# Kernel optimization log

Measured on AMD Instinct MI355X. Metric: run time of the kernel, lower is better.

Reference implementation:

```python
import jax, jax.numpy as jnp
import numpy as np

B, Z, K, T = 4, 64, 400, 48000
CIN, COUT, KS, DIL = 128, 128, 3, 1
H = 32


def setup_inputs() -> dict:
    key = jax.random.key(0)
    ks = jax.random.split(key, 10)
    s = lambda n: 1.0 / np.sqrt(n)
    return {
        "x": jax.random.normal(ks[0], (B, CIN, T), jnp.float32),
        "z": jax.random.normal(ks[1], (B, Z, K), jnp.float32),
        # weight_model: Conv1d(Z->H, k=1), ReLU, Conv1d(H -> CIN*COUT*KS, k=1)
        "w1": jax.random.normal(ks[2], (H, Z), jnp.float32) * s(Z),
        "b1": jax.random.normal(ks[3], (H,), jnp.float32) * 0.01,
        "w2": jax.random.normal(ks[4], (CIN * COUT * KS, H), jnp.float32) * s(H),
        "b2": jax.random.normal(ks[5], (CIN * COUT * KS,), jnp.float32) * s(CIN * KS),
        # bias_model: Conv1d(Z->H, k=1), ReLU, Conv1d(H -> COUT, k=1)
        "bw1": jax.random.normal(ks[6], (H, Z), jnp.float32) * s(Z),
        "bb1": jax.random.normal(ks[7], (H,), jnp.float32) * 0.01,
        "bw2": jax.random.normal(ks[8], (COUT, H), jnp.float32) * s(H),
        "bb2": jax.random.normal(ks[9], (COUT,), jnp.float32) * 0.01,
    }


def _mlp1x1(z, wa, ba, wb, bb):
    # two pointwise Conv1d layers with ReLU in between; z: [B, Z, K]
    h = jax.nn.relu(jnp.einsum('hz,bzk->bhk', wa, z) + ba[None, :, None])
    return jnp.einsum('oh,bhk->bok', wb, h) + bb[None, :, None]


def _unfold_causal(x, ksize, dil):
    # causal im2col: tap i is x delayed by i*dil samples (left-padded with zeros)
    pad = dil * (ksize - 1)
    xp = jnp.pad(x, ((0, 0), (0, 0), (pad, 0)))
    taps = [xp[:, :, pad - i * dil: pad - i * dil + x.shape[-1]] for i in range(ksize)]
    return jnp.concatenate(taps, axis=1)  # [B, CIN*KS, T]


def reference(x, z, w1, b1, w2, b2, bw1, bb1, bw2, bb2):
    Tk = T // K  # samples per weight chunk
    xu = _unfold_causal(x, KS, DIL)                       # [B, CIN*KS, T]
    xr = xu.transpose(0, 2, 1).reshape(B * K, Tk, CIN * KS)
    w = _mlp1x1(z, w1, b1, w2, b2)                        # [B, CIN*COUT*KS, K]
    w = w.reshape(B, CIN * KS, COUT, K).transpose(0, 3, 1, 2).reshape(B * K, CIN * KS, COUT)
    bias = _mlp1x1(z, bw1, bb1, bw2, bb2)                 # [B, COUT, K]
    bias = bias.transpose(0, 2, 1).reshape(B * K, COUT)
    y = jnp.einsum('btc,bco->bto', xr, w) + bias[:, None, :]
    return y.reshape(B, T, COUT).transpose(0, 2, 1)       # [B, COUT, T]
```

## Files before the change

kernel.cpp:

```cpp
#include <hip/hip_runtime.h>
#include <stdint.h>

#define TT     48000
#define TK     120
#define NC     128
#define NA     384
#define NZ     64
#define NH     32
#define NK     400
#define NCHUNK 1600
#define MW     49152
#define XROWS  48002

typedef float f32x4 __attribute__((ext_vector_type(4)));
typedef __bf16 bf16x8 __attribute__((ext_vector_type(8)));

static __device__ __forceinline__ uint16_t f2bf(float f) {
    uint32_t x; __builtin_memcpy(&x, &f, 4);
    return (uint16_t)((x + 0x7fffu + ((x >> 16) & 1u)) >> 16);
}
static __device__ __forceinline__ uint32_t pk2(uint16_t lo, uint16_t hi) {
    return (uint32_t)lo | ((uint32_t)hi << 16);
}

__global__ __launch_bounds__(256) void k0w(
    const float* __restrict__ w2, const float* __restrict__ b2,
    uint16_t* __restrict__ w2p, float* __restrict__ b2p) {
    int m = blockIdx.x * 256 + threadIdx.x;
    int a = m >> 7, c = m & 127;
    int mp = c * NA + a;
    const float* src = w2 + (size_t)m * NH;
    uint16_t* dst = w2p + (size_t)mp * NH;
#pragma unroll
    for (int i = 0; i < NH; i += 8) {
        float4 v0 = *(const float4*)(src + i);
        float4 v1 = *(const float4*)(src + i + 4);
        uint4 o;
        o.x = pk2(f2bf(v0.x), f2bf(v0.y));
        o.y = pk2(f2bf(v0.z), f2bf(v0.w));
        o.z = pk2(f2bf(v1.x), f2bf(v1.y));
        o.w = pk2(f2bf(v1.z), f2bf(v1.w));
        *(uint4*)(dst + i) = o;
    }
    b2p[mp] = b2[m];
}

__global__ __launch_bounds__(256) void k0x(
    const float* __restrict__ x, uint16_t* __restrict__ Xt) {
    int t0 = blockIdx.x * 128, cin0 = blockIdx.y * 64, b = blockIdx.z;
    int tid = threadIdx.x;
    __shared__ __align__(16) uint16_t Lt[128][72];
    const float* xb = x + ((size_t)b * NC + cin0) * TT + t0;
    int cg = (tid & 7) * 8;
    int tq = (tid >> 3) * 4;
    uint16_t vb[4][8];
#pragma unroll
    for (int i = 0; i < 8; ++i) {
        float4 v = *(const float4*)(xb + (size_t)(cg + i) * TT + tq);
        vb[0][i] = f2bf(v.x); vb[1][i] = f2bf(v.y);
        vb[2][i] = f2bf(v.z); vb[3][i] = f2bf(v.w);
    }
#pragma unroll
    for (int j = 0; j < 4; ++j) {
        uint4 o; __builtin_memcpy(&o, vb[j], 16);
        *(uint4*)&Lt[tq + j][cg] = o;
    }
    __syncthreads();
    uint16_t* XtB = Xt + (size_t)b * XROWS * NC;
#pragma unroll
    for (int r = 0; r < 4; ++r) {
        int s = r * 256 + tid;
        int t = s >> 3, cc = s & 7;
        uint4 o = *(uint4*)&Lt[t][cc * 8];
        *(uint4*)(XtB + (size_t)(t0 + t + 2) * NC + cin0 + cc * 8) = o;
    }
    if (blockIdx.x == 0 && blockIdx.y == 0 && tid < 32)
        *(uint4*)(XtB + tid * 8) = make_uint4(0, 0, 0, 0);
}

__global__ __launch_bounds__(256) void k1_hidden(
    const float* __restrict__ z,
    const float* __restrict__ w1, const float* __restrict__ b1,
    const float* __restrict__ bw1, const float* __restrict__ bb1,
    const float* __restrict__ bw2, const float* __restrict__ bb2,
    uint16_t* __restrict__ Hb, float* __restrict__ biasws) {
    int tid = threadIdx.x, lane = tid & 63, w = tid >> 6;
    int chunk0 = blockIdx.x * 4;
    int b = chunk0 / NK;
    int k0 = chunk0 - b * NK;

    __shared__ float w1sT[64][33];
    __shared__ float bw1sT[64][33];
    __shared__ float bw2s[128][33];
    __shared__ float zs[64][4];
    __shared__ float hbs[4][33];
    __shared__ float b1s[32], bb1s[32], bb2s[128];

    {
        int row = tid >> 3, c0 = (tid & 7) * 8;
        float4 a0 = *(const float4*)(w1 + row * NZ + c0);
        float4 a1 = *(const float4*)(w1 + row * NZ + c0 + 4);
        float4 c0v = *(const float4*)(bw1 + row * NZ + c0);
        float4 c1v = *(const float4*)(bw1 + row * NZ + c0 + 4);
        const float av[8] = {a0.x,a0.y,a0.z,a0.w,a1.x,a1.y,a1.z,a1.w};
        const float cv[8] = {c0v.x,c0v.y,c0v.z,c0v.w,c1v.x,c1v.y,c1v.z,c1v.w};
#pragma unroll
        for (int j = 0; j < 8; ++j) {
            w1sT[c0 + j][row]  = av[j];
            bw1sT[c0 + j][row] = cv[j];
        }
    }
    {
        int r = tid >> 1, cb = (tid & 1) * 16;
        float4 v0 = *(const float4*)(bw2 + r * NH + cb);
        float4 v1 = *(const float4*)(bw2 + r * NH + cb + 4);
        float4 v2 = *(const float4*)(bw2 + r * NH + cb + 8);
        float4 v3 = *(const float4*)(bw2 + r * NH + cb + 12);
        const float vv[16] = {v0.x,v0.y,v0.z,v0.w,v1.x,v1.y,v1.z,v1.w,
                              v2.x,v2.y,v2.z,v2.w,v3.x,v3.y,v3.z,v3.w};
#pragma unroll
        for (int j = 0; j < 16; ++j) bw2s[r][cb + j] = vv[j];
    }
    if (tid < 64) {
        float4 zv = *(const float4*)(z + ((size_t)b * NZ + tid) * NK + k0);
        zs[tid][0] = zv.x; zs[tid][1] = zv.y; zs[tid][2] = zv.z; zs[tid][3] = zv.w;
    }
    if (tid < 32) { b1s[tid] = b1[tid]; bb1s[tid] = bb1[tid]; }
    if (tid >= 128 && tid < 256) bb2s[tid - 128] = bb2[tid - 128];
    __syncthreads();

    int chunk = chunk0 + w;
    if (lane < NH) {
        float s = b1s[lane];
#pragma unroll
        for (int i = 0; i < NZ; ++i) s = fmaf(w1sT[i][lane], zs[i][w], s);
        Hb[(size_t)chunk * NH + lane] = f2bf(fmaxf(s, 0.f));
    } else {
        int j = lane - NH;
        float s = bb1s[j];
#pragma unroll
        for (int i = 0; i < NZ; ++i) s = fmaf(bw1sT[i][j], zs[i][w], s);
        hbs[w][j] = fmaxf(s, 0.f);
    }

#pragma unroll
    for (int r = 0; r < 2; ++r) {
        int c = r * 64 + lane;
        float s = bb2s[c];
#pragma unroll
        for (int j = 0; j < NH; ++j) s = fmaf(bw2s[c][j], hbs[w][j], s);
        biasws[(size_t)chunk * NC + c] = s;
    }
}

__global__ __launch_bounds__(256) void k2_wgen(
    const uint16_t* __restrict__ w2p, const float* __restrict__ b2p,
    const uint16_t* __restrict__ Hb, uint16_t* __restrict__ Wt,
    int chunk0, int nchunk) {
    int tid = threadIdx.x, lane = tid & 63, w = tid >> 6;
    int quad = lane >> 4, li = lane & 15;
    __shared__ __align__(16) uint16_t St[4][16][264];

    int clocal = blockIdx.y * 16 + li;
    int cl = clocal < nchunk ? clocal : (nchunk - 1);
    bf16x8 bfrag = *(const bf16x8*)(Hb + (size_t)(chunk0 + cl) * NH + quad * 8);
    int mbase = blockIdx.x * 1024 + w * 256;

#pragma unroll
    for (int t = 0; t < 16; ++t) {
        int mb = mbase + t * 16;
        bf16x8 afrag = *(const bf16x8*)(w2p + (size_t)(mb + li) * NH + quad * 8);
        f32x4 acc = {0.f, 0.f, 0.f, 0.f};
        acc = __builtin_amdgcn_mfma_f32_16x16x32_bf16(afrag, bfrag, acc, 0, 0, 0);
        float4 bias = *(const float4*)(b2p + mb + quad * 4);
        uint16_t p[4] = { f2bf(acc[0] + bias.x), f2bf(acc[1] + bias.y),
                          f2bf(acc[2] + bias.z), f2bf(acc[3] + bias.w) };
        uint64_t pv; __builtin_memcpy(&pv, p, 8);
        *(uint64_t*)&St[w][li][t * 16 + quad * 4] = pv;
    }
#pragma unroll
    for (int p = 0; p < 8; ++p) {
        int ch = (lane >> 4) + (p & 3) * 4;
        int part = lane & 15, mh = p >> 2;
        uint4 v = *(const uint4*)&St[w][ch][mh * 128 + part * 8];
        int cg = blockIdx.y * 16 + ch;
        if (cg < nchunk)
            *(uint4*)(Wt + (size_t)cg * MW + mbase + mh * 128 + part * 8) = v;
    }
}

__global__ __launch_bounds__(256) void k3_conv(
    const uint16_t* __restrict__ Xt, const uint16_t* __restrict__ Wt,
    const float* __restrict__ biasws, float* __restrict__ out, int chunk0) {
    int cl = blockIdx.x, chunk = chunk0 + cl;
    int b = chunk / NK, k = chunk - b * NK;
    int kbase = k * TK;
    int tid = threadIdx.x, lane = tid & 63, w = tid >> 6;
    int quad = lane >> 4, li = lane & 15;
    int tblk = (w & 1) * 64, cblk = (w >> 1) * 64;

    __shared__ __align__(16) char smem[49152];
    char* Xa = smem;
    char* Ws = smem + 32768;
    const uint16_t* XtB = Xt + (size_t)b * XROWS * NC;
    const uint16_t* WtC = Wt + (size_t)cl * MW;

    f32x4 acc[4][4];
#pragma unroll
    for (int i = 0; i < 4; ++i)
#pragma unroll
        for (int j = 0; j < 4; ++j) acc[i][j] = (f32x4){0.f, 0.f, 0.f, 0.f};

#pragma unroll
    for (int i = 0; i < 8; ++i) {
        int brow = w * 32 + i * 4 + quad;
        const uint16_t* g = XtB + (size_t)(kbase + brow) * NC
                          + ((li ^ (brow & 15)) * 8);
        __builtin_amdgcn_global_load_lds(
            (__attribute__((address_space(1))) void*)g,
            (__attribute__((address_space(3))) void*)(Xa + (w * 32 + i * 4) * 256),
            16, 0, 0);
    }

    {
        int a0 = 0;
#pragma unroll
        for (int i = 0; i < 4; ++i) {
            int kc = 2 * w + (i >> 1), half = i & 1;
            int c = half * 64 + lane;
            const uint16_t* g = WtC + (size_t)c * NA + a0 + kc * 8;
            __builtin_amdgcn_global_load_lds(
                (__attribute__((address_space(1))) void*)g,
                (__attribute__((address_space(3))) void*)(Ws + kc * 2048 + half * 1024),
                16, 0, 0);
        }
    }
    __syncthreads();

#pragma unroll
    for (int dk = 0; dk < 6; ++dk) {
        int tap = dk >> 1;
#pragma unroll
        for (int s = 0; s < 2; ++s) {
            bf16x8 af[4], bfr[4];
#pragma unroll
            for (int tt = 0; tt < 4; ++tt) {
                int r = tblk + tt * 16 + li + 2 - tap;
                r = r > 127 ? 127 : r;
                int q = (dk & 1) * 8 + s * 4 + quad;
                af[tt] = *(const bf16x8*)(Xa + r * 256 + ((q ^ (r & 15)) << 4));
            }
#pragma unroll
            for (int ct = 0; ct < 4; ++ct)
                bfr[ct] = *(const bf16x8*)(Ws + (s * 4 + quad) * 2048 + (cblk + ct * 16 + li) * 16);
#pragma unroll
            for (int tt = 0; tt < 4; ++tt)
#pragma unroll
                for (int ct = 0; ct < 4; ++ct)
                    acc[tt][ct] = __builtin_amdgcn_mfma_f32_16x16x32_bf16(
                        af[tt], bfr[ct], acc[tt][ct], 0, 0, 0);
        }
        __syncthreads();
        if (dk < 5) {
            int a0 = (dk + 1) * 64;
#pragma unroll
            for (int i = 0; i < 4; ++i) {
                int kc = 2 * w + (i >> 1), half = i & 1;
                int c = half * 64 + lane;
                const uint16_t* g = WtC + (size_t)c * NA + a0 + kc * 8;
                __builtin_amdgcn_global_load_lds(
                    (__attribute__((address_space(1))) void*)g,
                    (__attribute__((address_space(3))) void*)(Ws + kc * 2048 + half * 1024),
                    16, 0, 0);
            }
            __syncthreads();
        }
    }

#pragma unroll
    for (int ct = 0; ct < 4; ++ct) {
        int c = cblk + ct * 16 + li;
        float bias = biasws[(size_t)chunk * NC + c];
        float* ob = out + ((size_t)b * NC + c) * TT + kbase;
#pragma unroll
        for (int tt = 0; tt < 4; ++tt) {
            int t0v = tblk + tt * 16 + quad * 4;
            if (t0v < TK) {
                f32x4 v = acc[tt][ct];
                *(float4*)(ob + t0v) = make_float4(v[0] + bias, v[1] + bias,
                                                   v[2] + bias, v[3] + bias);
            }
        }
    }
}

extern "C" void kernel_launch(void* const* d_in, const int* in_sizes, int n_in,
                              void* d_out, int out_size, void* d_ws, size_t ws_size,
                              hipStream_t stream) {
    const float* x   = (const float*)d_in[0];
    const float* z   = (const float*)d_in[1];
    const float* w1  = (const float*)d_in[2];
    const float* b1  = (const float*)d_in[3];
    const float* w2  = (const float*)d_in[4];
    const float* b2  = (const float*)d_in[5];
    const float* bw1 = (const float*)d_in[6];
    const float* bb1 = (const float*)d_in[7];
    const float* bw2 = (const float*)d_in[8];
    const float* bb2 = (const float*)d_in[9];
    float* out = (float*)d_out;

    char* ws = (char*)d_ws;
    uint16_t* Hb     = (uint16_t*)(ws);
    float*    biasws = (float*)(ws + 102400);
    uint16_t* w2p    = (uint16_t*)(ws + 921600);
    float*    b2p    = (float*)(ws + 4067328);
    uint16_t* Xt     = (uint16_t*)(ws + 4263936);
    const size_t wt_off = 53422080;
    uint16_t* Wt     = (uint16_t*)(ws + wt_off);

    size_t avail = (ws_size > wt_off) ? (ws_size - wt_off) : 0;
    int batch = (int)(avail / ((size_t)MW * 2));
    if (batch > 800) batch = 800;
    if (batch < 1) batch = 1;

    k0w<<<MW / 256, 256, 0, stream>>>(w2, b2, w2p, b2p);
    k0x<<<dim3(TT / 128, 2, 4), 256, 0, stream>>>(x, Xt);
    k1_hidden<<<NCHUNK / 4, 256, 0, stream>>>(z, w1, b1, bw1, bb1, bw2, bb2, Hb, biasws);

    for (int c0 = 0; c0 < NCHUNK; c0 += batch) {
        int nc = NCHUNK - c0;
        if (nc > batch) nc = batch;
        dim3 g2(MW / 1024, (nc + 15) / 16, 1);
        k2_wgen<<<g2, 256, 0, stream>>>(w2p, b2p, Hb, Wt, c0, nc);
        k3_conv<<<nc, 256, 0, stream>>>(Xt, Wt, biasws, out, c0);
    }
}
```

Baseline: 310.0 us.

## Double-buffer weight slices in LDS with swizzled layout and one barrier per step

```diff
diff --git a/kernel.cpp b/kernel.cpp
--- a/kernel.cpp
+++ b/kernel.cpp
@@ -199,9 +199,10 @@
     int quad = lane >> 4, li = lane & 15;
     int tblk = (w & 1) * 64, cblk = (w >> 1) * 64;
 
-    __shared__ __align__(16) char smem[49152];
-    char* Xa = smem;
-    char* Ws = smem + 32768;
+    __shared__ __align__(16) char smem[65536];
+    char* Xa  = smem;
+    char* Db0 = smem + 32768;
+    char* Db1 = smem + 49152;
     const uint16_t* XtB = Xt + (size_t)b * XROWS * NC;
     const uint16_t* WtC = Wt + (size_t)cl * MW;
 
@@ -210,6 +211,20 @@
     for (int i = 0; i < 4; ++i)
 #pragma unroll
         for (int j = 0; j < 4; ++j) acc[i][j] = (f32x4){0.f, 0.f, 0.f, 0.f};
+
+    auto stageD = [&](char* dst, int dks) {
+#pragma unroll
+        for (int j = 0; j < 4; ++j) {
+            int g = (w * 4 + j) * 64 + lane;
+            int c = g >> 3, sd = g & 7;
+            int o = sd ^ (c & 7);
+            const uint16_t* gsrc = WtC + (size_t)c * NA + dks * 64 + o * 8;
+            __builtin_amdgcn_global_load_lds(
+                (__attribute__((address_space(1))) void*)gsrc,
+                (__attribute__((address_space(3))) void*)(dst + (w * 4 + j) * 1024),
+                16, 0, 0);
+        }
+    };
 
 #pragma unroll
     for (int i = 0; i < 8; ++i) {
@@ -221,28 +236,27 @@
             (__attribute__((address_space(3))) void*)(Xa + (w * 32 + i * 4) * 256),
             16, 0, 0);
     }
-
-    {
-        int a0 = 0;
-#pragma unroll
-        for (int i = 0; i < 4; ++i) {
-            int kc = 2 * w + (i >> 1), half = i & 1;
-            int c = half * 64 + lane;
-            const uint16_t* g = WtC + (size_t)c * NA + a0 + kc * 8;
-            __builtin_amdgcn_global_load_lds(
-                (__attribute__((address_space(1))) void*)g,
-                (__attribute__((address_space(3))) void*)(Ws + kc * 2048 + half * 1024),
-                16, 0, 0);
-        }
-    }
-    __syncthreads();
+    stageD(Db0, 0);
 
 #pragma unroll
     for (int dk = 0; dk < 6; ++dk) {
+        __syncthreads();
+        if (dk < 5) stageD((dk & 1) ? Db0 : Db1, dk + 1);
+        char* cur = (dk & 1) ? Db1 : Db0;
         int tap = dk >> 1;
+
+        bf16x8 bfr[2][4];
+#pragma unroll
+        for (int s = 0; s < 2; ++s)
+#pragma unroll
+            for (int ct = 0; ct < 4; ++ct) {
+                int c = cblk + ct * 16 + li;
+                bfr[s][ct] = *(const bf16x8*)(cur + c * 128
+                             + (((s * 4 + quad) ^ (c & 7)) << 4));
+            }
 #pragma unroll
         for (int s = 0; s < 2; ++s) {
-            bf16x8 af[4], bfr[4];
+            bf16x8 af[4];
 #pragma unroll
             for (int tt = 0; tt < 4; ++tt) {
                 int r = tblk + tt * 16 + li + 2 - tap;
@@ -251,29 +265,11 @@
                 af[tt] = *(const bf16x8*)(Xa + r * 256 + ((q ^ (r & 15)) << 4));
             }
 #pragma unroll
-            for (int ct = 0; ct < 4; ++ct)
-                bfr[ct] = *(const bf16x8*)(Ws + (s * 4 + quad) * 2048 + (cblk + ct * 16 + li) * 16);
-#pragma unroll
             for (int tt = 0; tt < 4; ++tt)
 #pragma unroll
                 for (int ct = 0; ct < 4; ++ct)
                     acc[tt][ct] = __builtin_amdgcn_mfma_f32_16x16x32_bf16(
-                        af[tt], bfr[ct], acc[tt][ct], 0, 0, 0);
-        }
-        __syncthreads();
-        if (dk < 5) {
-            int a0 = (dk + 1) * 64;
-#pragma unroll
-            for (int i = 0; i < 4; ++i) {
-                int kc = 2 * w + (i >> 1), half = i & 1;
-                int c = half * 64 + lane;
-                const uint16_t* g = WtC + (size_t)c * NA + a0 + kc * 8;
-                __builtin_amdgcn_global_load_lds(
-                    (__attribute__((address_space(1))) void*)g,
-                    (__attribute__((address_space(3))) void*)(Ws + kc * 2048 + half * 1024),
-                    16, 0, 0);
-            }
-            __syncthreads();
+                        af[tt], bfr[s][ct], acc[tt][ct], 0, 0, 0);
         }
     }
 
```

After: 302.8 us. -2.3%, faster.
